# Optimization experiments

Hardware: AMD Instinct MI355X
Metric: run time of the kernel (lower is better)

Reference implementation:

```python
import jax, jax.numpy as jnp
import numpy as np

MARGIN = 1.0

def masked_maximum(data, mask, axis=1):
    axis_min = jnp.min(data, axis=axis, keepdims=True)
    return jnp.max((data - axis_min) * mask, axis=axis, keepdims=True) + axis_min

def masked_minimum(data, mask, axis=1):
    axis_max = jnp.max(data, axis=axis, keepdims=True)
    return jnp.min((data - axis_max) * mask, axis=axis, keepdims=True) + axis_max

def setup_inputs() -> dict:
    key = jax.random.key(0)
    k1, k2 = jax.random.split(key)
    B = 512
    pdist_matrix = jax.random.uniform(k1, (B, B), dtype=jnp.float32)
    target = jax.random.randint(k2, (B,), 0, 64, dtype=jnp.int64)
    return {"pdist_matrix": pdist_matrix, "target": target}

def reference(pdist_matrix, target):
    B = pdist_matrix.shape[0]
    labels = target.astype(jnp.int32)[:, None]                    # [B,1]
    adjacency = labels == labels.T                                # [B,B] bool
    adjacency_not = ~adjacency

    # Tile pdist over anchor-positive pairs: [B*B, B]
    pdist_tile = jnp.tile(pdist_matrix, (B, 1))
    # mask[i*B+j, k] = (label[j] != label[k]) & (d(j,k) > d(j,i))
    mask = jnp.tile(adjacency_not, (B, 1)) & (
        pdist_tile > pdist_matrix.T.reshape(-1, 1))
    mask_final = (jnp.sum(mask.astype(jnp.float32), axis=1, keepdims=True)
                  > 0.0).reshape(B, B).T                          # [B,B]

    adjacency_not_f = adjacency_not.astype(jnp.float32)
    mask_f = mask.astype(jnp.float32)

    negatives_outside = masked_minimum(pdist_tile, mask_f).reshape(B, B).T
    negatives_inside = jnp.tile(
        masked_maximum(pdist_matrix, adjacency_not_f), (1, B))    # [B,B]
    semi_hard_negatives = jnp.where(mask_final, negatives_outside,
                                    negatives_inside)

    loss_mat = MARGIN + pdist_matrix - semi_hard_negatives
    mask_positives = adjacency.astype(jnp.float32) - jnp.eye(B, dtype=jnp.float32)
    num_positives = jnp.maximum(jnp.sum(mask_positives), 1.0)
    triplet_loss = jnp.sum(jnp.maximum(loss_mat * mask_positives, 0.0)) / num_positives
    return triplet_loss
```

## Files before the change

kernel.cpp:

```cpp
#include <hip/hip_runtime.h>
#include <math.h>

#define BB 512

__global__ __launch_bounds__(256) void tshl_row_kernel(
    const float* __restrict__ pdist, const int* __restrict__ target,
    float* __restrict__ row_sum, float* __restrict__ row_cnt)
{
    const int lane = threadIdx.x & 63;
    const int w    = threadIdx.x >> 6;
    const int j    = (blockIdx.x << 2) + w;

    const int base = lane << 3;
    const float4 p0 = *(const float4*)(pdist + j * BB + base);
    const float4 p1 = *(const float4*)(pdist + j * BB + base + 4);
    const int4   t0 = *(const int4*)(target + base);
    const int4   t1 = *(const int4*)(target + base + 4);
    const int myLab = target[j];

    const float d[8]   = {p0.x, p0.y, p0.z, p0.w, p1.x, p1.y, p1.z, p1.w};
    const int   lab[8] = {t0.x, t0.y, t0.z, t0.w, t1.x, t1.y, t1.z, t1.w};

    bool neg[8], pos[8];
    float lmax = -INFINITY, lmin = INFINITY;
    #pragma unroll
    for (int u = 0; u < 8; ++u) {
        neg[u] = (lab[u] != myLab);
        pos[u] = (!neg[u]) && (base + u != j);
        lmin = fminf(lmin, d[u]);
        if (neg[u]) lmax = fmaxf(lmax, d[u]);
    }
    #pragma unroll
    for (int m = 32; m; m >>= 1) {
        lmax = fmaxf(lmax, __shfl_xor(lmax, m));
        lmin = fminf(lmin, __shfl_xor(lmin, m));
    }
    const float neg_in = (lmax == -INFINITY) ? lmin : lmax;

    float psum = 0.0f;
    int   npos = 0;
    #pragma unroll
    for (int u = 0; u < 8; ++u) {
        unsigned long long bal = __ballot(pos[u]);
        npos += __popcll(bal);
        while (bal) {
            const int src = __builtin_ctzll(bal);
            bal &= bal - 1;
            const float dpos = __shfl(d[u], src);
            float c = INFINITY;
            #pragma unroll
            for (int v = 0; v < 8; ++v)
                if (neg[v] && d[v] > dpos) c = fminf(c, d[v]);
            #pragma unroll
            for (int m = 32; m; m >>= 1) c = fminf(c, __shfl_xor(c, m));
            const float shn = (c < INFINITY) ? c : neg_in;
            psum += fmaxf(1.0f + dpos - shn, 0.0f);
        }
    }

    if (lane == 0) {
        row_sum[j] = psum;
        row_cnt[j] = (float)npos;
    }
}

__global__ __launch_bounds__(64) void tshl_final_kernel(
    const float* __restrict__ row_sum, const float* __restrict__ row_cnt,
    float* __restrict__ out)
{
    const int lane = threadIdx.x;
    const int base = lane << 3;
    const float4 s0 = *(const float4*)(row_sum + base);
    const float4 s1 = *(const float4*)(row_sum + base + 4);
    const float4 c0 = *(const float4*)(row_cnt + base);
    const float4 c1 = *(const float4*)(row_cnt + base + 4);
    float s = ((s0.x + s0.y) + (s0.z + s0.w)) + ((s1.x + s1.y) + (s1.z + s1.w));
    float c = ((c0.x + c0.y) + (c0.z + c0.w)) + ((c1.x + c1.y) + (c1.z + c1.w));
    #pragma unroll
    for (int m = 32; m; m >>= 1) {
        s += __shfl_xor(s, m);
        c += __shfl_xor(c, m);
    }
    if (lane == 0) out[0] = s / fmaxf(c, 1.0f);
}

extern "C" void kernel_launch(void* const* d_in, const int* in_sizes, int n_in,
                              void* d_out, int out_size, void* d_ws, size_t ws_size,
                              hipStream_t stream) {
    const float* pdist  = (const float*)d_in[0];
    const int*   target = (const int*)d_in[1];
    float* ws      = (float*)d_ws;
    float* row_sum = ws;
    float* row_cnt = ws + BB;
    float* out     = (float*)d_out;

    tshl_row_kernel<<<BB / 4, 256, 0, stream>>>(pdist, target, row_sum, row_cnt);
    tshl_final_kernel<<<1, 64, 0, stream>>>(row_sum, row_cnt, out);
}
```

Baseline: 13.28 us.

## Fuse final reduction into row kernel via last-block atomic counter

Merges the two-kernel pipeline into one launch. Each block now handles 8 rows with 512 threads, reduces its partial sums in shared memory and publishes them. An atomic ticket counter lets the last-arriving block do the final reduction and write the loss. This removes the second kernel launch and its dependency gap. The counter is never reset, so correctness depends on it starting at zero and the modulo check lining up across repeated calls.

```diff
diff --git a/kernel.cpp b/kernel.cpp
--- a/kernel.cpp
+++ b/kernel.cpp
@@ -1,15 +1,18 @@
 #include <hip/hip_runtime.h>
 #include <math.h>
 
-#define BB 512
+#define BB   512
+#define NBLK 64
+#define TPB  512
 
-__global__ __launch_bounds__(256) void tshl_row_kernel(
+__global__ __launch_bounds__(TPB) void tshl_kernel(
     const float* __restrict__ pdist, const int* __restrict__ target,
-    float* __restrict__ row_sum, float* __restrict__ row_cnt)
+    float* __restrict__ part_sum, float* __restrict__ part_cnt,
+    unsigned int* __restrict__ counter, float* __restrict__ out)
 {
     const int lane = threadIdx.x & 63;
     const int w    = threadIdx.x >> 6;
-    const int j    = (blockIdx.x << 2) + w;
+    const int j    = (blockIdx.x << 3) + w;
 
     const int base = lane << 3;
     const float4 p0 = *(const float4*)(pdist + j * BB + base);
@@ -58,30 +61,43 @@
         }
     }
 
-    if (lane == 0) {
-        row_sum[j] = psum;
-        row_cnt[j] = (float)npos;
+    __shared__ float ssum[8], scnt[8];
+    if (lane == 0) { ssum[w] = psum; scnt[w] = (float)npos; }
+    __syncthreads();
+
+    unsigned int old = 0;
+    if (threadIdx.x == 0) {
+        float bs = 0.0f, bc = 0.0f;
+        #pragma unroll
+        for (int e = 0; e < 8; ++e) { bs += ssum[e]; bc += scnt[e]; }
+        __hip_atomic_store(&part_sum[blockIdx.x], bs, __ATOMIC_RELAXED,
+                           __HIP_MEMORY_SCOPE_AGENT);
+        __hip_atomic_store(&part_cnt[blockIdx.x], bc, __ATOMIC_RELAXED,
+                           __HIP_MEMORY_SCOPE_AGENT);
+        __threadfence();
+        old = __hip_atomic_fetch_add(counter, 1u, __ATOMIC_RELEASE,
+                                     __HIP_MEMORY_SCOPE_AGENT);
     }
-}
 
-__global__ __launch_bounds__(64) void tshl_final_kernel(
-    const float* __restrict__ row_sum, const float* __restrict__ row_cnt,
-    float* __restrict__ out)
-{
-    const int lane = threadIdx.x;
-    const int base = lane << 3;
-    const float4 s0 = *(const float4*)(row_sum + base);
-    const float4 s1 = *(const float4*)(row_sum + base + 4);
-    const float4 c0 = *(const float4*)(row_cnt + base);
-    const float4 c1 = *(const float4*)(row_cnt + base + 4);
-    float s = ((s0.x + s0.y) + (s0.z + s0.w)) + ((s1.x + s1.y) + (s1.z + s1.w));
-    float c = ((c0.x + c0.y) + (c0.z + c0.w)) + ((c1.x + c1.y) + (c1.z + c1.w));
-    #pragma unroll
-    for (int m = 32; m; m >>= 1) {
-        s += __shfl_xor(s, m);
-        c += __shfl_xor(c, m);
+    if (w == 0) {
+        old = __shfl(old, 0);
+        if ((old & (NBLK - 1)) == (NBLK - 1)) {
+            __threadfence();
+            float s = 0.0f, c = 0.0f;
+            if (lane < NBLK) {
+                s = __hip_atomic_load(&part_sum[lane], __ATOMIC_RELAXED,
+                                      __HIP_MEMORY_SCOPE_AGENT);
+                c = __hip_atomic_load(&part_cnt[lane], __ATOMIC_RELAXED,
+                                      __HIP_MEMORY_SCOPE_AGENT);
+            }
+            #pragma unroll
+            for (int m = 32; m; m >>= 1) {
+                s += __shfl_xor(s, m);
+                c += __shfl_xor(c, m);
+            }
+            if (lane == 0) out[0] = s / fmaxf(c, 1.0f);
+        }
     }
-    if (lane == 0) out[0] = s / fmaxf(c, 1.0f);
 }
 
 extern "C" void kernel_launch(void* const* d_in, const int* in_sizes, int n_in,
@@ -89,11 +105,12 @@
                               hipStream_t stream) {
     const float* pdist  = (const float*)d_in[0];
     const int*   target = (const int*)d_in[1];
-    float* ws      = (float*)d_ws;
-    float* row_sum = ws;
-    float* row_cnt = ws + BB;
-    float* out     = (float*)d_out;
+    float* ws             = (float*)d_ws;
+    float* part_sum       = ws;
+    float* part_cnt       = ws + NBLK;
+    unsigned int* counter = (unsigned int*)(ws + 2 * NBLK);
+    float* out            = (float*)d_out;
 
-    tshl_row_kernel<<<BB / 4, 256, 0, stream>>>(pdist, target, row_sum, row_cnt);
-    tshl_final_kernel<<<1, 64, 0, stream>>>(row_sum, row_cnt, out);
+    tshl_kernel<<<NBLK, TPB, 0, stream>>>(pdist, target, part_sum, part_cnt,
+                                          counter, out);
 }
```

Result: faster. 12.88 us (-3.0%).
